# Optimization experiments

Hardware: AMD Instinct MI355X
Metric: run time of the kernel (lower is better)

Reference implementation:

```python
import jax, jax.numpy as jnp
import numpy as np

INPUT, HIDDEN, PROJ = 4, 64, 49
B, T = 2048, 512


def setup_inputs() -> dict:
    key = jax.random.key(0)
    ks = jax.random.split(key, 8)
    s = 1.0 / np.sqrt(HIDDEN)
    u = lambda k, shape: jax.random.uniform(k, shape, jnp.float32, -s, s)
    return {
        "x": jax.random.normal(ks[0], (B, T, INPUT), jnp.float32),
        "W_ih": u(ks[1], (4 * HIDDEN, INPUT)),   # gates order i,f,g,o
        "W_hh": u(ks[2], (4 * HIDDEN, PROJ)),    # recurrent input is projected h (size PROJ)
        "b_ih": u(ks[3], (4 * HIDDEN,)),
        "b_hh": u(ks[4], (4 * HIDDEN,)),
        "W_hr": u(ks[5], (PROJ, HIDDEN)),        # projection h_full -> h
        "W_out": u(ks[6], (PROJ, PROJ)),         # final linear on last projected hidden state
        "b_out": u(ks[7], (PROJ,)),
    }


def reference(x, W_ih, W_hh, b_ih, b_hh, W_hr, W_out, b_out):
    Bx = x.shape[0]
    # precompute input contribution for all timesteps: [B, T, 4H]
    x_gates = jnp.einsum('bti,gi->btg', x, W_ih) + b_ih + b_hh

    def step(carry, xg_t):
        h, c = carry                      # h: [B, PROJ], c: [B, HIDDEN]
        gates = xg_t + h @ W_hh.T         # [B, 4H]
        i, f, g, o = jnp.split(gates, 4, axis=-1)
        i = jax.nn.sigmoid(i)
        f = jax.nn.sigmoid(f)
        g = jnp.tanh(g)
        o = jax.nn.sigmoid(o)
        c = f * c + i * g
        h_full = o * jnp.tanh(c)          # [B, HIDDEN]
        h = h_full @ W_hr.T               # [B, PROJ]
        return (h, c), None

    h0 = jnp.zeros((Bx, PROJ), x.dtype)
    c0 = jnp.zeros((Bx, HIDDEN), x.dtype)
    (h_last, _), _ = jax.lax.scan(step, (h0, c0), jnp.swapaxes(x_gates, 0, 1))
    return h_last @ W_out.T + b_out       # [B, PROJ]
```

## Files before the change

### kernel.cpp

```cpp
#include <hip/hip_runtime.h>

#define TSTEPS 512
#define BPB    4
#define ROWB   256
#define ABYTES (16 * ROWB)
#define KSTEPS 3

typedef short bf16x8 __attribute__((ext_vector_type(8)));
typedef float f32x4  __attribute__((ext_vector_type(4)));

__device__ __forceinline__ float fast_sigmoid(float x) {
    return __builtin_amdgcn_rcpf(1.0f + __expf(-x));
}
__device__ __forceinline__ float fast_tanh(float x) {
    return 1.0f - 2.0f * __builtin_amdgcn_rcpf(__expf(2.0f * x) + 1.0f);
}
__device__ __forceinline__ unsigned int f2bf(float f) {
    unsigned int u = __builtin_bit_cast(unsigned int, f);
    return (u + 0x7FFFu + ((u >> 16) & 1u)) >> 16;
}
__device__ __forceinline__ float bf2f(unsigned int us) {
    return __builtin_bit_cast(float, us << 16);
}
__device__ __forceinline__ unsigned int split_pack(float f) {
    unsigned int hi = f2bf(f);
    unsigned int lo = f2bf(f - bf2f(hi));
    return hi | (lo << 16);
}

__global__ __launch_bounds__(256, 2) void lstm_mfma5_kernel(
    const float* __restrict__ x,
    const float* __restrict__ W_ih,
    const float* __restrict__ W_hh,
    const float* __restrict__ b_ih,
    const float* __restrict__ b_hh,
    const float* __restrict__ W_hr,
    const float* __restrict__ W_out,
    const float* __restrict__ b_out,
    float* __restrict__ out)
{
    const int tid = threadIdx.x;
    const int w   = tid >> 6;
    const int l   = tid & 63;
    const int g4  = l >> 4;
    const int ln  = l & 15;
    const int b0  = blockIdx.x * BPB;

    __shared__ __align__(128) unsigned char Abuf[2 * ABYTES];
    __shared__ __align__(16)  float hf32[BPB][64];
    __shared__ float hproj[BPB][52];

    for (int i = tid; i < (2 * ABYTES) / 4; i += 256)
        ((unsigned int*)Abuf)[i] = 0u;
    __syncthreads();

    float Msum[4][16];
    #pragma unroll
    for (int t4 = 0; t4 < 4; ++t4)
        #pragma unroll
        for (int i = 0; i < 16; ++i) Msum[t4][i] = 0.0f;

    for (int p = 0; p < 49; ++p) {
        float wr[16];
        #pragma unroll
        for (int s = 0; s < 2; ++s)
            #pragma unroll
            for (int j = 0; j < 8; ++j)
                wr[s * 8 + j] = W_hr[p * 64 + s * 32 + g4 * 8 + j];
        #pragma unroll
        for (int t4 = 0; t4 < 4; ++t4) {
            const float whh = W_hh[(t4 * 64 + w * 16 + ln) * 49 + p];
            #pragma unroll
            for (int i = 0; i < 16; ++i) Msum[t4][i] += whh * wr[i];
        }
    }

    bf16x8 Bf[4][KSTEPS];
    union U { unsigned int d[4]; bf16x8 v; };
    #pragma unroll
    for (int t4 = 0; t4 < 4; ++t4) {
        #pragma unroll
        for (int s = 0; s < 2; ++s) {
            U u;
            #pragma unroll
            for (int jj = 0; jj < 4; ++jj) {
                const unsigned int e0 = f2bf(Msum[t4][s * 8 + 2 * jj]);
                const unsigned int e1 = f2bf(Msum[t4][s * 8 + 2 * jj + 1]);
                u.d[jj] = e0 | (e1 << 16);
            }
            Bf[t4][s] = u.v;
        }
        U u; u.d[0] = u.d[1] = u.d[2] = u.d[3] = 0u;
        const int n = t4 * 64 + w * 16 + ln;
        if (g4 == 0) {
            #pragma unroll
            for (int c = 0; c < 4; ++c) {
                const unsigned int us = f2bf(W_ih[n * 4 + c]);
                u.d[c] = us | (us << 16);
            }
        } else if (g4 == 1) {
            u.d[0] = f2bf(b_ih[n] + b_hh[n]);
        }
        Bf[t4][2] = u.v;
    }

    const bool xduty = ((tid & 15) == 0);
    int xbase = 0, xrowbyte = 0;
    float xw = 0.f, xn = 0.f;
    if (xduty) {
        const int v    = tid >> 4;
        const int bl   = v >> 2;
        const int comp = v & 3;
        const int row  = bl * 4;
        xbase    = (b0 + bl) * (TSTEPS * 4) + comp;
        xrowbyte = (row * ROWB + 128 + 4 * comp) ^ ((row & 7) << 4);
        *(unsigned int*)(Abuf + xrowbyte) = split_pack(x[xbase]);
        xw = x[xbase + 4 * 1];
        xn = x[xbase + 4 * 2];
    }
    if (tid < 32) {
        const int row = tid & 15, buf = tid >> 4;
        const int byte = (row * ROWB + 144) ^ ((row & 7) << 4);
        *(unsigned int*)(Abuf + buf * ABYTES + byte) = 0x3F80u;
    }
    __syncthreads();

    int aoff[KSTEPS];
    #pragma unroll
    for (int s = 0; s < KSTEPS; ++s)
        aoff[s] = (ln * ROWB + s * 64 + g4 * 16) ^ ((ln & 7) << 4);
    const int wrow  = g4 * 4;
    const int woff0 = (wrow * ROWB + 2 * (w * 16 + ln)) ^ ((wrow & 7) << 4);

    float cst = 0.f;
    float hffin = 0.f;
    int cur = 0;

    for (int t = 0; t < TSTEPS; ++t) {
        float xn2 = 0.0f;
        if (xduty) {
            const int tt = (t + 3 < TSTEPS) ? t + 3 : TSTEPS - 1;
            xn2 = x[xbase + 4 * tt];
        }

        const unsigned char* Ab = Abuf + cur * ABYTES;
        bf16x8 af[KSTEPS];
        #pragma unroll
        for (int s = 0; s < KSTEPS; ++s)
            af[s] = *(const bf16x8*)(Ab + aoff[s]);

        f32x4 aI = {0.f, 0.f, 0.f, 0.f}, aF = aI, aG = aI, aO = aI;
        #pragma unroll
        for (int s = 0; s < KSTEPS; ++s) {
            aI = __builtin_amdgcn_mfma_f32_16x16x32_bf16(af[s], Bf[0][s], aI, 0, 0, 0);
            aF = __builtin_amdgcn_mfma_f32_16x16x32_bf16(af[s], Bf[1][s], aF, 0, 0, 0);
            aG = __builtin_amdgcn_mfma_f32_16x16x32_bf16(af[s], Bf[2][s], aG, 0, 0, 0);
            aO = __builtin_amdgcn_mfma_f32_16x16x32_bf16(af[s], Bf[3][s], aO, 0, 0, 0);
        }

        unsigned char* An = Abuf + (cur ^ 1) * ABYTES;
        {
            const float gi = fast_sigmoid(aI[0]);
            const float gf = fast_sigmoid(aF[0]);
            const float gg = fast_tanh(aG[0]);
            const float go = fast_sigmoid(aO[0]);
            cst = gf * cst + gi * gg;
            const float hf = go * fast_tanh(cst);
            hffin = hf;
            *(unsigned short*)(An + woff0) = (unsigned short)f2bf(hf);
        }
        if (xduty)
            *(unsigned int*)(An + xrowbyte) = split_pack(xw);
        xw = xn; xn = xn2;

        __syncthreads();
        cur ^= 1;
    }

    hf32[g4][w * 16 + ln] = hffin;
    __syncthreads();

    for (int idx = tid; idx < BPB * 49; idx += 256) {
        const int bb = idx / 49, q = idx - bb * 49;
        float s = 0.0f;
        #pragma unroll 8
        for (int h = 0; h < 64; ++h) s += hf32[bb][h] * W_hr[q * 64 + h];
        hproj[bb][q] = s;
    }
    __syncthreads();
    for (int idx = tid; idx < BPB * 49; idx += 256) {
        const int bb = idx / 49, q2 = idx - bb * 49;
        float s = b_out[q2];
        #pragma unroll 7
        for (int p = 0; p < 49; ++p) s += hproj[bb][p] * W_out[q2 * 49 + p];
        out[(b0 + bb) * 49 + q2] = s;
    }
}

extern "C" void kernel_launch(void* const* d_in, const int* in_sizes, int n_in,
                              void* d_out, int out_size, void* d_ws, size_t ws_size,
                              hipStream_t stream) {
    (void)in_sizes; (void)n_in; (void)d_ws; (void)ws_size; (void)out_size;
    const float* x     = (const float*)d_in[0];
    const float* W_ih  = (const float*)d_in[1];
    const float* W_hh  = (const float*)d_in[2];
    const float* b_ih  = (const float*)d_in[3];
    const float* b_hh  = (const float*)d_in[4];
    const float* W_hr  = (const float*)d_in[5];
    const float* W_out = (const float*)d_in[6];
    const float* b_out = (const float*)d_in[7];
    float* outp = (float*)d_out;

    lstm_mfma5_kernel<<<dim3(2048 / BPB), dim3(256), 0, stream>>>(
        x, W_ih, W_hh, b_ih, b_hh, W_hr, W_out, b_out, outp);
}
```

Before: 224.0 us.

## Fold exp2 scaling into gate weights, pack h stores, stagger block start

Pre-scales the gate weights, input weights and biases by -log2(e) (or 2*log2(e) for the g gate), so each activation becomes a raw exp2 plus a reciprocal with no multiply on the critical per-step path. Pairs adjacent lanes via a shuffle so h is written to shared memory as one 32-bit store per lane pair instead of two 16-bit stores. Adds a short s_sleep on half the blocks to stagger co-resident blocks, and manually unrolls the MFMA chain. Scaling before bf16 rounding slightly changes the rounding error, and the shuffle adds a cross-lane op to each step.

```diff
diff --git a/kernel.cpp b/kernel.cpp
--- a/kernel.cpp
+++ b/kernel.cpp
@@ -4,17 +4,11 @@
 #define BPB    4
 #define ROWB   256
 #define ABYTES (16 * ROWB)
-#define KSTEPS 3
+#define LOG2E  1.44269504088896340736f
 
 typedef short bf16x8 __attribute__((ext_vector_type(8)));
 typedef float f32x4  __attribute__((ext_vector_type(4)));
 
-__device__ __forceinline__ float fast_sigmoid(float x) {
-    return __builtin_amdgcn_rcpf(1.0f + __expf(-x));
-}
-__device__ __forceinline__ float fast_tanh(float x) {
-    return 1.0f - 2.0f * __builtin_amdgcn_rcpf(__expf(2.0f * x) + 1.0f);
-}
 __device__ __forceinline__ unsigned int f2bf(float f) {
     unsigned int u = __builtin_bit_cast(unsigned int, f);
     return (u + 0x7FFFu + ((u >> 16) & 1u)) >> 16;
@@ -27,8 +21,11 @@
     unsigned int lo = f2bf(f - bf2f(hi));
     return hi | (lo << 16);
 }
-
-__global__ __launch_bounds__(256, 2) void lstm_mfma5_kernel(
+__device__ __forceinline__ float rcp1p(float e) {
+    return __builtin_amdgcn_rcpf(1.0f + e);
+}
+
+__global__ __launch_bounds__(256, 2) void lstm_mfma10_kernel(
     const float* __restrict__ x,
     const float* __restrict__ W_ih,
     const float* __restrict__ W_hh,
@@ -75,17 +72,18 @@
         }
     }
 
-    bf16x8 Bf[4][KSTEPS];
+    bf16x8 Bf[4][3];
     union U { unsigned int d[4]; bf16x8 v; };
     #pragma unroll
     for (int t4 = 0; t4 < 4; ++t4) {
+        const float fac = (t4 == 2) ? 2.0f * LOG2E : -LOG2E;
         #pragma unroll
         for (int s = 0; s < 2; ++s) {
             U u;
             #pragma unroll
             for (int jj = 0; jj < 4; ++jj) {
-                const unsigned int e0 = f2bf(Msum[t4][s * 8 + 2 * jj]);
-                const unsigned int e1 = f2bf(Msum[t4][s * 8 + 2 * jj + 1]);
+                const unsigned int e0 = f2bf(fac * Msum[t4][s * 8 + 2 * jj]);
+                const unsigned int e1 = f2bf(fac * Msum[t4][s * 8 + 2 * jj + 1]);
                 u.d[jj] = e0 | (e1 << 16);
             }
             Bf[t4][s] = u.v;
@@ -94,12 +92,12 @@
         const int n = t4 * 64 + w * 16 + ln;
         if (g4 == 0) {
             #pragma unroll
-            for (int c = 0; c < 4; ++c) {
-                const unsigned int us = f2bf(W_ih[n * 4 + c]);
-                u.d[c] = us | (us << 16);
+            for (int c4 = 0; c4 < 4; ++c4) {
+                const unsigned int us = f2bf(fac * W_ih[n * 4 + c4]);
+                u.d[c4] = us | (us << 16);
             }
         } else if (g4 == 1) {
-            u.d[0] = f2bf(b_ih[n] + b_hh[n]);
+            u.d[0] = f2bf(fac * (b_ih[n] + b_hh[n]));
         }
         Bf[t4][2] = u.v;
     }
@@ -125,12 +123,17 @@
     }
     __syncthreads();
 
-    int aoff[KSTEPS];
+    if ((blockIdx.x ^ (blockIdx.x >> 8)) & 1) {
+        __builtin_amdgcn_s_sleep(8);
+        __builtin_amdgcn_s_sleep(1);
+    }
+
+    int aoff[3];
     #pragma unroll
-    for (int s = 0; s < KSTEPS; ++s)
+    for (int s = 0; s < 3; ++s)
         aoff[s] = (ln * ROWB + s * 64 + g4 * 16) ^ ((ln & 7) << 4);
     const int wrow  = g4 * 4;
-    const int woff0 = (wrow * ROWB + 2 * (w * 16 + ln)) ^ ((wrow & 7) << 4);
+    const int woffp = (wrow * ROWB + 2 * (w * 16 + ln)) ^ ((wrow & 7) << 4);
 
     float cst = 0.f;
     float hffin = 0.f;
@@ -144,30 +147,39 @@
         }
 
         const unsigned char* Ab = Abuf + cur * ABYTES;
-        bf16x8 af[KSTEPS];
-        #pragma unroll
-        for (int s = 0; s < KSTEPS; ++s)
-            af[s] = *(const bf16x8*)(Ab + aoff[s]);
+        const bf16x8 af0 = *(const bf16x8*)(Ab + aoff[0]);
+        const bf16x8 af1 = *(const bf16x8*)(Ab + aoff[1]);
+        const bf16x8 af2 = *(const bf16x8*)(Ab + aoff[2]);
 
         f32x4 aI = {0.f, 0.f, 0.f, 0.f}, aF = aI, aG = aI, aO = aI;
-        #pragma unroll
-        for (int s = 0; s < KSTEPS; ++s) {
-            aI = __builtin_amdgcn_mfma_f32_16x16x32_bf16(af[s], Bf[0][s], aI, 0, 0, 0);
-            aF = __builtin_amdgcn_mfma_f32_16x16x32_bf16(af[s], Bf[1][s], aF, 0, 0, 0);
-            aG = __builtin_amdgcn_mfma_f32_16x16x32_bf16(af[s], Bf[2][s], aG, 0, 0, 0);
-            aO = __builtin_amdgcn_mfma_f32_16x16x32_bf16(af[s], Bf[3][s], aO, 0, 0, 0);
-        }
+        aI = __builtin_amdgcn_mfma_f32_16x16x32_bf16(af0, Bf[0][0], aI, 0, 0, 0);
+        aF = __builtin_amdgcn_mfma_f32_16x16x32_bf16(af0, Bf[1][0], aF, 0, 0, 0);
+        aG = __builtin_amdgcn_mfma_f32_16x16x32_bf16(af0, Bf[2][0], aG, 0, 0, 0);
+        aO = __builtin_amdgcn_mfma_f32_16x16x32_bf16(af0, Bf[3][0], aO, 0, 0, 0);
+        aI = __builtin_amdgcn_mfma_f32_16x16x32_bf16(af1, Bf[0][1], aI, 0, 0, 0);
+        aF = __builtin_amdgcn_mfma_f32_16x16x32_bf16(af1, Bf[1][1], aF, 0, 0, 0);
+        aG = __builtin_amdgcn_mfma_f32_16x16x32_bf16(af1, Bf[2][1], aG, 0, 0, 0);
+        aO = __builtin_amdgcn_mfma_f32_16x16x32_bf16(af1, Bf[3][1], aO, 0, 0, 0);
+        aI = __builtin_amdgcn_mfma_f32_16x16x32_bf16(af2, Bf[0][2], aI, 0, 0, 0);
+        aF = __builtin_amdgcn_mfma_f32_16x16x32_bf16(af2, Bf[1][2], aF, 0, 0, 0);
+        aG = __builtin_amdgcn_mfma_f32_16x16x32_bf16(af2, Bf[2][2], aG, 0, 0, 0);
+        aO = __builtin_amdgcn_mfma_f32_16x16x32_bf16(af2, Bf[3][2], aO, 0, 0, 0);
 
         unsigned char* An = Abuf + (cur ^ 1) * ABYTES;
         {
-            const float gi = fast_sigmoid(aI[0]);
-            const float gf = fast_sigmoid(aF[0]);
-            const float gg = fast_tanh(aG[0]);
-            const float go = fast_sigmoid(aO[0]);
-            cst = gf * cst + gi * gg;
-            const float hf = go * fast_tanh(cst);
+            const float gi = rcp1p(__builtin_amdgcn_exp2f(aI[0]));
+            const float gf = rcp1p(__builtin_amdgcn_exp2f(aF[0]));
+            const float rg = rcp1p(__builtin_amdgcn_exp2f(aG[0]));
+            const float gg = fmaf(-2.0f, rg, 1.0f);
+            const float go = rcp1p(__builtin_amdgcn_exp2f(aO[0]));
+            cst = fmaf(gf, cst, gi * gg);
+            const float rc = rcp1p(__builtin_amdgcn_exp2f(cst * (2.0f * LOG2E)));
+            const float hf = go * fmaf(-2.0f, rc, 1.0f);
             hffin = hf;
-            *(unsigned short*)(An + woff0) = (unsigned short)f2bf(hf);
+            const unsigned int ub = f2bf(hf);
+            const unsigned int up = __shfl_xor(ub, 1);
+            if (!(ln & 1))
+                *(unsigned int*)(An + woffp) = ub | (up << 16);
         }
         if (xduty)
             *(unsigned int*)(An + xrowbyte) = split_pack(xw);
@@ -211,6 +223,6 @@
     const float* b_out = (const float*)d_in[7];
     float* outp = (float*)d_out;
 
-    lstm_mfma5_kernel<<<dim3(2048 / BPB), dim3(256), 0, stream>>>(
+    lstm_mfma10_kernel<<<dim3(2048 / BPB), dim3(256), 0, stream>>>(
         x, W_ih, W_hh, b_ih, b_hh, W_hr, W_out, b_out, outp);
 }
```

Measured after the change: 246.9 us. 10.2% more time.
